# Kernel optimization log

Hardware: AMD Instinct MI355X
Metric: run time of the kernel (lower is better)

Reference implementation:

```python
import jax, jax.numpy as jnp
import numpy as np

N_HEADS = 16
D_HEAD = 64
D_MODEL = 1024
WINDOW = 256
B, T = 4, 2048


def rotate_half(x):
    x1, x2 = jnp.split(x, 2, axis=-1)
    return jnp.concatenate([-x2, x1], axis=-1)


def apply_rope(x, cos, sin):
    return x * cos + rotate_half(x) * sin


def setup_inputs() -> dict:
    key = jax.random.key(0)
    ks = jax.random.split(key, 5)
    x = jax.random.normal(ks[0], (B, T, D_MODEL), dtype=jnp.float32)
    cos = jax.random.normal(ks[1], (1, T, 1, D_HEAD), dtype=jnp.float32)
    sin = jax.random.normal(ks[2], (1, T, 1, D_HEAD), dtype=jnp.float32)
    qkv_w = jax.random.normal(ks[3], (3 * D_MODEL, D_MODEL), dtype=jnp.float32) * (D_MODEL ** -0.5)
    out_w = jax.random.normal(ks[4], (D_MODEL, D_MODEL), dtype=jnp.float32) * (D_MODEL ** -0.5)
    return {"x": x, "cos": cos, "sin": sin, "qkv_w": qkv_w, "out_w": out_w}


def reference(x, cos, sin, qkv_w, out_w):
    Bc, Tc, C = x.shape
    # QKV projection (bias-free Linear: y = x @ W^T)
    qkv = jnp.einsum('btc,fc->btf', x, qkv_w)
    q, k, v = jnp.split(qkv, 3, axis=-1)
    # [B, H, T, d]
    def to_heads(t):
        return t.reshape(Bc, Tc, N_HEADS, D_HEAD).transpose(0, 2, 1, 3)
    q, k, v = to_heads(q), to_heads(k), to_heads(v)
    # RoPE: cos/sin [1, T, 1, d] -> [1, 1, T, d] broadcasting over heads
    cos_t = cos[:, :Tc].transpose(0, 2, 1, 3)
    sin_t = sin[:, :Tc].transpose(0, 2, 1, 3)
    q = apply_rope(q, cos_t, sin_t)
    k = apply_rope(k, cos_t, sin_t)
    # banded causal mask: allow j <= i and j >= i - (window-1)
    i = jnp.arange(Tc)[:, None]
    j = jnp.arange(Tc)[None, :]
    allowed = (j <= i) & (j >= i - (WINDOW - 1))  # [T, T]
    scale = 1.0 / jnp.sqrt(jnp.asarray(D_HEAD, dtype=q.dtype))
    scores = jnp.einsum('bhqd,bhkd->bhqk', q, k) * scale
    scores = jnp.where(allowed[None, None], scores, jnp.finfo(scores.dtype).min)
    attn = jax.nn.softmax(scores, axis=-1)
    out = jnp.einsum('bhqk,bhkd->bhqd', attn, v)
    out = out.transpose(0, 2, 1, 3).reshape(Bc, Tc, C)
    return jnp.einsum('btc,oc->bto', out, out_w)
```

## Files before the change

kernel.cpp:

```cpp
#include <hip/hip_runtime.h>

typedef __bf16 bf16_t;
typedef __bf16 bf16x8 __attribute__((ext_vector_type(8)));
typedef __bf16 bf16x4 __attribute__((ext_vector_type(4)));
typedef float f32x4 __attribute__((ext_vector_type(4)));

#define GLOAD_LDS16(gptr, lptr)                                                              \
  __builtin_amdgcn_global_load_lds((const __attribute__((address_space(1))) void*)(gptr),    \
                                   (__attribute__((address_space(3))) void*)(lptr), 16, 0, 0)

__device__ __forceinline__ f32x4 f32x4_zero() {
  f32x4 v; v[0] = 0.f; v[1] = 0.f; v[2] = 0.f; v[3] = 0.f; return v;
}

__device__ __forceinline__ int kxr(int r) { return (r & 7) ^ (((r >> 3) & 3) << 1); }

__device__ __forceinline__ void rope8(const bf16x8 xl, const bf16x8 xh,
                                      const float* __restrict__ cosb,
                                      const float* __restrict__ sinb, float sc,
                                      bf16x8& ol, bf16x8& oh) {
  float4 cl0 = *(const float4*)(cosb);
  float4 cl1 = *(const float4*)(cosb + 4);
  float4 ch0 = *(const float4*)(cosb + 32);
  float4 ch1 = *(const float4*)(cosb + 36);
  float4 sl0 = *(const float4*)(sinb);
  float4 sl1 = *(const float4*)(sinb + 4);
  float4 sh0 = *(const float4*)(sinb + 32);
  float4 sh1 = *(const float4*)(sinb + 36);
  float cl[8] = {cl0.x, cl0.y, cl0.z, cl0.w, cl1.x, cl1.y, cl1.z, cl1.w};
  float ch[8] = {ch0.x, ch0.y, ch0.z, ch0.w, ch1.x, ch1.y, ch1.z, ch1.w};
  float sl[8] = {sl0.x, sl0.y, sl0.z, sl0.w, sl1.x, sl1.y, sl1.z, sl1.w};
  float sh[8] = {sh0.x, sh0.y, sh0.z, sh0.w, sh1.x, sh1.y, sh1.z, sh1.w};
#pragma unroll
  for (int e = 0; e < 8; e++) {
    float a = (float)xl[e], b = (float)xh[e];
    ol[e] = (bf16_t)((a * cl[e] - b * sl[e]) * sc);
    oh[e] = (bf16_t)((b * ch[e] + a * sh[e]) * sc);
  }
}

__global__ void cast3_kernel(const float* __restrict__ a, const float* __restrict__ b,
                             const float* __restrict__ c, bf16_t* __restrict__ oa,
                             bf16_t* __restrict__ ob, bf16_t* __restrict__ oc) {
  int i = blockIdx.x * blockDim.x + threadIdx.x;
  const float* src; bf16_t* dst; int j;
  if (i < 2097152) { src = a; dst = oa; j = i; }
  else if (i < 2883584) { src = b; dst = ob; j = i - 2097152; }
  else { src = c; dst = oc; j = i - 2883584; }
  float4 v = ((const float4*)src)[j];
  bf16x4 o;
  o[0] = (bf16_t)v.x; o[1] = (bf16_t)v.y; o[2] = (bf16_t)v.z; o[3] = (bf16_t)v.w;
  ((bf16x4*)dst)[j] = o;
}

template <int MODE>
__global__ __launch_bounds__(256) void gemm_bt_kernel(
    const bf16_t* __restrict__ A, const bf16_t* __restrict__ B, float* __restrict__ C,
    bf16_t* __restrict__ oq, bf16_t* __restrict__ ok_, bf16_t* __restrict__ ov,
    int M, int N, int K) {
  constexpr int BM = 128, BN = 128, BK = 32;
  __shared__ bf16_t As[BM * BK];
  __shared__ bf16_t Bs[BN * BK];
  const int tid = threadIdx.x;
  const int lane = tid & 63;
  const int wid = tid >> 6;
  const int wm = (wid >> 1) * 64;
  const int wn = (wid & 1) * 64;
  const int l16 = lane & 15;
  const int qd = lane >> 4;
  const int bm = blockIdx.x, bn = blockIdx.y;

  const int srow = tid >> 2;
  const int skol = (tid & 3) * 8;

  const bf16_t* gA = A + (size_t)(bm * BM + srow) * K + skol;
  const bf16_t* gB = B + (size_t)(bn * BN + srow) * K + skol;
  bf16_t* lA = &As[srow * BK + skol];
  bf16_t* lB = &Bs[srow * BK + skol];

  f32x4 acc[4][4];
#pragma unroll
  for (int mb = 0; mb < 4; mb++)
#pragma unroll
    for (int nb = 0; nb < 4; nb++) acc[mb][nb] = f32x4_zero();

  for (int k0 = 0; k0 < K; k0 += BK) {
    __syncthreads();
    GLOAD_LDS16(gA + k0, lA);
    GLOAD_LDS16(gA + (size_t)64 * K + k0, lA + 64 * BK);
    GLOAD_LDS16(gB + k0, lB);
    GLOAD_LDS16(gB + (size_t)64 * K + k0, lB + 64 * BK);
    __syncthreads();

    bf16x8 af[4], bfr[4];
#pragma unroll
    for (int mb = 0; mb < 4; mb++)
      af[mb] = *(const bf16x8*)&As[(wm + mb * 16 + l16) * BK + qd * 8];
#pragma unroll
    for (int nb = 0; nb < 4; nb++)
      bfr[nb] = *(const bf16x8*)&Bs[(wn + nb * 16 + l16) * BK + qd * 8];
#pragma unroll
    for (int mb = 0; mb < 4; mb++)
#pragma unroll
      for (int nb = 0; nb < 4; nb++)
        acc[mb][nb] = __builtin_amdgcn_mfma_f32_16x16x32_bf16(af[mb], bfr[nb], acc[mb][nb], 0, 0, 0);
  }

  if (MODE == 0) {
#pragma unroll
    for (int mb = 0; mb < 4; mb++)
#pragma unroll
      for (int nb = 0; nb < 4; nb++)
#pragma unroll
        for (int r = 0; r < 4; r++) {
          int row = bm * BM + wm + mb * 16 + qd * 4 + r;
          int col = bn * BN + wn + nb * 16 + l16;
          C[(size_t)row * N + col] = acc[mb][nb][r];
        }
  } else {
    const int part = bn >> 3;
    const int h = ((bn * 128 + wn) & 1023) >> 6;
    bf16_t* dst = (part == 0) ? oq : (part == 1) ? ok_ : ov;
#pragma unroll
    for (int mb = 0; mb < 4; mb++)
#pragma unroll
      for (int r = 0; r < 4; r++) {
        int row = bm * BM + wm + mb * 16 + qd * 4 + r;
        int b = row >> 11, t = row & 2047;
        size_t basei = (((size_t)(b * 16 + h)) * 2048 + t) * 64;
#pragma unroll
        for (int nb = 0; nb < 4; nb++)
          dst[basei + nb * 16 + l16] = (bf16_t)acc[mb][nb][r];
      }
  }
}

__global__ __launch_bounds__(256) void attn_kernel(
    const bf16_t* __restrict__ qh, const bf16_t* __restrict__ kh,
    const bf16_t* __restrict__ vh, bf16_t* __restrict__ ao,
    const float* __restrict__ cosp, const float* __restrict__ sinp) {
  __shared__ bf16_t qs[64 * 64];
  __shared__ bf16_t ks[64 * 64];
  __shared__ bf16_t vs[64 * 64];
  __shared__ bf16_t vswz[8 * 64 * 8];
  __shared__ bf16_t ps[4][16 * 64];

  const int tid = threadIdx.x;
  const int lane = tid & 63;
  const int wid = tid >> 6;
  const int l16 = lane & 15;
  const int qd = lane >> 4;

  const int bh = blockIdx.x;
  const int i0 = blockIdx.y * 64;
  const int b = bh >> 4, h = bh & 15;

  auto swz4 = [](int f) { int r = f >> 3; return r * 8 + ((f & 7) ^ (r & 7)); };
  const int r0 = tid >> 3, q0 = tid & 7;
  const int rr = tid >> 2, qo = tid & 3;

  {
    const bf16x8* src = (const bf16x8*)(qh + ((size_t)bh * 2048 + i0) * 64);
    bf16x8* dst = (bf16x8*)qs;
    const int fl = rr * 8 + qo, fh = fl + 4;
    bf16x8 ol, oh;
    rope8(src[fl], src[fh], cosp + (i0 + rr) * 64 + qo * 8, sinp + (i0 + rr) * 64 + qo * 8,
          0.18033688011112042f, ol, oh);
    dst[swz4(fl)] = ol;
    dst[swz4(fh)] = oh;
  }

  bf16x8 bones;
#pragma unroll
  for (int e = 0; e < 8; e++) bones[e] = (bf16_t)1.0f;

  float l_i[4] = {0.f, 0.f, 0.f, 0.f};
  f32x4 oacc[4];
#pragma unroll
  for (int nb = 0; nb < 4; nb++) oacc[nb] = f32x4_zero();

  const int c1 = i0 >> 6;
  const int c0 = (c1 >= 4) ? (c1 - 4) : 0;

  for (int c = c0; c <= c1; c++) {
    const int j0 = c * 64;
    __syncthreads();
    {
      const bf16x8* ksrc = (const bf16x8*)(kh + ((size_t)bh * 2048 + j0) * 64);
      const uint4* vsrc = (const uint4*)(vh + ((size_t)bh * 2048 + j0) * 64);
      bf16x8* kdst = (bf16x8*)ks;
      uint4* vdst = (uint4*)vs;
      const int fl = rr * 8 + qo, fh = fl + 4;
      bf16x8 ol, oh;
      rope8(ksrc[fl], ksrc[fh], cosp + (j0 + rr) * 64 + qo * 8, sinp + (j0 + rr) * 64 + qo * 8,
            1.0f, ol, oh);
      kdst[swz4(fl)] = ol;
      kdst[swz4(fh)] = oh;
      vdst[r0 * 8 + (q0 ^ kxr(r0))] = vsrc[tid];
      vdst[(r0 + 32) * 8 + (q0 ^ kxr(r0 + 32))] = vsrc[tid + 256];
    }
    __syncthreads();

    f32x4 sacc[4];
#pragma unroll
    for (int nb = 0; nb < 4; nb++) sacc[nb] = f32x4_zero();
#pragma unroll
    for (int kk = 0; kk < 2; kk++) {
      bf16x8 afr = *(const bf16x8*)&qs[(wid * 16 + l16) * 64 + (((kk * 4 + qd) ^ (l16 & 7)) * 8)];
#pragma unroll
      for (int nb = 0; nb < 4; nb++) {
        bf16x8 bfr = *(const bf16x8*)&ks[(nb * 16 + l16) * 64 + (((kk * 4 + qd) ^ (l16 & 7)) * 8)];
        sacc[nb] = __builtin_amdgcn_mfma_f32_16x16x32_bf16(afr, bfr, sacc[nb], 0, 0, 0);
      }
    }

#pragma unroll
    for (int p2 = 0; p2 < 2; p2++) {
      int combo = p2 * 4 + wid;
      int jbase = (combo >> 2) * 32 + (lane >> 4) * 8;
      int dcol = (combo & 3) * 16 + (lane & 15);
      int bb = dcol >> 3, dlo = dcol & 7;
      bf16x8 v8;
#pragma unroll
      for (int e = 0; e < 8; e++) {
        int row = jbase + e;
        v8[e] = vs[row * 64 + ((bb ^ kxr(row)) * 8) + dlo];
      }
      *(bf16x8*)&vswz[(combo * 64 + lane) * 8] = v8;
    }

#pragma unroll
    for (int r = 0; r < 4; r++) {
      const int i = i0 + wid * 16 + qd * 4 + r;
      const int prow = qd * 4 + r;
#pragma unroll
      for (int nb = 0; nb < 4; nb++) {
        const int j = j0 + nb * 16 + l16;
        bool valid = (j <= i) && (j + 256 > i);
        float p = valid ? exp2f(sacc[nb][r]) : 0.f;
        ps[wid][prow * 64 + (((nb * 2 + (l16 >> 3)) ^ (prow & 7)) * 8) + (l16 & 7)] = (bf16_t)p;
      }
    }

    __syncthreads();

    f32x4 lacc = f32x4_zero();
#pragma unroll
    for (int kk = 0; kk < 2; kk++) {
      bf16x8 afr = *(const bf16x8*)&ps[wid][l16 * 64 + (((kk * 4 + qd) ^ (l16 & 7)) * 8)];
      lacc = __builtin_amdgcn_mfma_f32_16x16x32_bf16(afr, bones, lacc, 0, 0, 0);
#pragma unroll
      for (int nb = 0; nb < 4; nb++) {
        bf16x8 bfr = *(const bf16x8*)&vswz[((kk * 4 + nb) * 64 + lane) * 8];
        oacc[nb] = __builtin_amdgcn_mfma_f32_16x16x32_bf16(afr, bfr, oacc[nb], 0, 0, 0);
      }
    }
#pragma unroll
    for (int r = 0; r < 4; r++) l_i[r] += lacc[r];
  }

#pragma unroll
  for (int nb = 0; nb < 4; nb++) {
#pragma unroll
    for (int r = 0; r < 4; r++) {
      int t = i0 + wid * 16 + qd * 4 + r;
      ao[((size_t)(b * 2048 + t)) * 1024 + h * 64 + nb * 16 + l16] =
          (bf16_t)(oacc[nb][r] / l_i[r]);
    }
  }
}

extern "C" void kernel_launch(void* const* d_in, const int* in_sizes, int n_in,
                              void* d_out, int out_size, void* d_ws, size_t ws_size,
                              hipStream_t stream) {
  const float* x    = (const float*)d_in[0];
  const float* cosp = (const float*)d_in[1];
  const float* sinp = (const float*)d_in[2];
  const float* qkvw = (const float*)d_in[3];
  const float* outw = (const float*)d_in[4];
  float* out = (float*)d_out;

  char* ws = (char*)d_ws;
  bf16_t* xb  = (bf16_t*)(ws + 0);
  bf16_t* qwb = (bf16_t*)(ws + 16777216);
  bf16_t* owb = (bf16_t*)(ws + 23068672);
  bf16_t* qhp = (bf16_t*)(ws + 25165824);
  bf16_t* khp = (bf16_t*)(ws + 41943040);
  bf16_t* vhp = (bf16_t*)(ws + 58720256);
  bf16_t* aop = (bf16_t*)(ws + 75497472);

  cast3_kernel<<<12288, 256, 0, stream>>>(x, qkvw, outw, xb, qwb, owb);

  gemm_bt_kernel<1><<<dim3(64, 24), 256, 0, stream>>>(xb, qwb, nullptr, qhp, khp, vhp,
                                                      8192, 3072, 1024);
  attn_kernel<<<dim3(64, 32), 256, 0, stream>>>(qhp, khp, vhp, aop, cosp, sinp);
  gemm_bt_kernel<0><<<dim3(64, 8), 256, 0, stream>>>(aop, owb, out, nullptr, nullptr, nullptr,
                                                     8192, 1024, 1024);
}
```

Before: 244.7 us.

## Precompute K RoPE in separate kernel and register-prefetch next K/V tile

Moves RoPE on K out of the attention inner loop into a standalone pass that rewrites K in place once, so each K tile is no longer rotated repeatedly by the up to five query blocks that read it. The attention loop now loads the next K/V tile into registers while the current one is computed, overlapping global loads with MFMA work. This adds an extra kernel launch and a full read/write pass over K, plus more register pressure in the attention kernel.

```diff
diff --git a/kernel.cpp b/kernel.cpp
--- a/kernel.cpp
+++ b/kernel.cpp
@@ -53,6 +53,21 @@
   ((bf16x4*)dst)[j] = o;
 }
 
+__global__ __launch_bounds__(256) void rope_k_kernel(bf16_t* __restrict__ kh,
+                                                     const float* __restrict__ cosp,
+                                                     const float* __restrict__ sinp) {
+  int idx = blockIdx.x * 256 + threadIdx.x;
+  int qo = idx & 3;
+  int row = idx >> 2;
+  int t = row & 2047;
+  bf16x8* base = (bf16x8*)(kh + (size_t)row * 64);
+  bf16x8 lo = base[qo], hi = base[qo + 4];
+  bf16x8 ol, oh;
+  rope8(lo, hi, cosp + t * 64 + qo * 8, sinp + t * 64 + qo * 8, 1.0f, ol, oh);
+  base[qo] = ol;
+  base[qo + 4] = oh;
+}
+
 template <int MODE>
 __global__ __launch_bounds__(256) void gemm_bt_kernel(
     const bf16_t* __restrict__ A, const bf16_t* __restrict__ B, float* __restrict__ C,
@@ -181,23 +196,32 @@
 
   const int c1 = i0 >> 6;
   const int c0 = (c1 >= 4) ? (c1 - 4) : 0;
+  const size_t bhbase = (size_t)bh * 2048;
+
+  uint4 kr0, kr1, vr0, vr1;
+  {
+    const uint4* ksrc = (const uint4*)(kh + (bhbase + (size_t)c0 * 64) * 64);
+    const uint4* vsrc = (const uint4*)(vh + (bhbase + (size_t)c0 * 64) * 64);
+    kr0 = ksrc[tid]; kr1 = ksrc[tid + 256];
+    vr0 = vsrc[tid]; vr1 = vsrc[tid + 256];
+  }
 
   for (int c = c0; c <= c1; c++) {
     const int j0 = c * 64;
     __syncthreads();
     {
-      const bf16x8* ksrc = (const bf16x8*)(kh + ((size_t)bh * 2048 + j0) * 64);
-      const uint4* vsrc = (const uint4*)(vh + ((size_t)bh * 2048 + j0) * 64);
-      bf16x8* kdst = (bf16x8*)ks;
+      uint4* kdst = (uint4*)ks;
       uint4* vdst = (uint4*)vs;
-      const int fl = rr * 8 + qo, fh = fl + 4;
-      bf16x8 ol, oh;
-      rope8(ksrc[fl], ksrc[fh], cosp + (j0 + rr) * 64 + qo * 8, sinp + (j0 + rr) * 64 + qo * 8,
-            1.0f, ol, oh);
-      kdst[swz4(fl)] = ol;
-      kdst[swz4(fh)] = oh;
-      vdst[r0 * 8 + (q0 ^ kxr(r0))] = vsrc[tid];
-      vdst[(r0 + 32) * 8 + (q0 ^ kxr(r0 + 32))] = vsrc[tid + 256];
+      kdst[swz4(tid)] = kr0;
+      kdst[swz4(tid + 256)] = kr1;
+      vdst[r0 * 8 + (q0 ^ kxr(r0))] = vr0;
+      vdst[(r0 + 32) * 8 + (q0 ^ kxr(r0 + 32))] = vr1;
+    }
+    if (c < c1) {
+      const uint4* ksrc = (const uint4*)(kh + (bhbase + (size_t)(c + 1) * 64) * 64);
+      const uint4* vsrc = (const uint4*)(vh + (bhbase + (size_t)(c + 1) * 64) * 64);
+      kr0 = ksrc[tid]; kr1 = ksrc[tid + 256];
+      vr0 = vsrc[tid]; vr1 = vsrc[tid + 256];
     }
     __syncthreads();
 
@@ -293,6 +317,7 @@
 
   gemm_bt_kernel<1><<<dim3(64, 24), 256, 0, stream>>>(xb, qwb, nullptr, qhp, khp, vhp,
                                                       8192, 3072, 1024);
+  rope_k_kernel<<<2048, 256, 0, stream>>>(khp, cosp, sinp);
   attn_kernel<<<dim3(64, 32), 256, 0, stream>>>(qhp, khp, vhp, aop, cosp, sinp);
   gemm_bt_kernel<0><<<dim3(64, 8), 256, 0, stream>>>(aop, owb, out, nullptr, nullptr, nullptr,
                                                      8192, 1024, 1024);
```

Result: no change. 241.3 us (-1.4%).
